# Performance work log

Measured on AMD Instinct MI355X. Metric: run time of the kernel, lower is better.

## Reference

```python
import jax, jax.numpy as jnp
import numpy as np
import math

B, N, D_MODEL, D_QK, D_V = 8, 2048, 512, 64, 64
NEG_INF = float('-inf')

def setup_inputs() -> dict:
    key = jax.random.key(0)
    k1, k2, k3, k4, k5 = jax.random.split(key, 5)
    mask = jax.random.randint(k1, (B, N, N), 0, 2).astype(bool)
    x_key_value = jax.random.normal(k2, (B, N, D_MODEL), dtype=jnp.float32)
    wk = jax.random.normal(k3, (D_MODEL, D_QK), dtype=jnp.float32) * 0.02
    wq = jax.random.normal(k4, (D_MODEL, D_QK), dtype=jnp.float32) * 0.02
    wv = jax.random.normal(k5, (D_MODEL, D_V), dtype=jnp.float32) * 0.02
    return {"mask": mask, "x_key_value": x_key_value, "wk": wk, "wq": wq, "wv": wv}

def reference(mask, x_key_value, wk, wq, wv):
    # self-attention: x_query defaults to x_key_value
    div = math.sqrt(wk.shape[1])
    k = x_key_value @ wk          # [n, j, d_qk]
    q = x_key_value @ wq          # [n, i, d_qk]
    v = x_key_value @ wv          # [n, j, d_v]
    mat = jnp.einsum('nik,njk->nij', q, k) / div
    mat = jnp.where(mask, mat, NEG_INF)
    portion = jax.nn.softmax(mat, axis=2)
    return jnp.einsum('nij,njk->nik', portion, v)
```

## Files before the change

### kernel.cpp

```cpp
#include <hip/hip_runtime.h>
#include <hip/hip_bf16.h>

typedef __attribute__((ext_vector_type(8))) short bf16x8;
typedef __attribute__((ext_vector_type(4))) float f32x4;
typedef __hip_bfloat16 bf16;

#define BATCH 8
#define SEQ   2048
#define DMODEL 512
#define DHEAD 64
#define ROWS (BATCH * SEQ)
#define SCALE_LOG2 0.1803368801f

static __device__ inline short f2bf(float f) {
    union { __hip_bfloat16 h; short s; } u;
    u.h = __float2bfloat16(f);
    return u.s;
}

__global__ __launch_bounds__(256) void transpose_w_kernel(
    const float* __restrict__ wq, const float* __restrict__ wk,
    const float* __restrict__ wv, bf16* __restrict__ wt)
{
    const int s  = blockIdx.x / 8;
    const int kt = blockIdx.x % 8;
    const float* w = (s == 0) ? wq : ((s == 1) ? wk : wv);

    __shared__ float Ts[64][68];

    const int tid = threadIdx.x;
    int nr = tid >> 4;
    int n4 = (tid & 15) * 4;
#pragma unroll
    for (int p = 0; p < 4; ++p) {
        int k = 16 * p + nr;
        float4 v = *(const float4*)(w + (size_t)(kt * 64 + k) * DHEAD + n4);
        Ts[k][n4] = v.x; Ts[k][n4 + 1] = v.y; Ts[k][n4 + 2] = v.z; Ts[k][n4 + 3] = v.w;
    }
    __syncthreads();
#pragma unroll
    for (int p = 0; p < 2; ++p) {
        int cc = tid + p * 256;
        int n = cc >> 3;
        int kk = (cc & 7) * 8;
        bf16x8 o;
#pragma unroll
        for (int e = 0; e < 8; ++e) o[e] = f2bf(Ts[kk + e][n]);
        *(bf16x8*)(wt + (size_t)(s * 64 + n) * DMODEL + kt * 64 + kk) = o;
    }
}

__global__ __launch_bounds__(512, 4) void proj_kernel(
    const float* __restrict__ x, const bf16* __restrict__ wt,
    bf16* __restrict__ Q, bf16* __restrict__ K, bf16* __restrict__ Vt)
{
    const int r0 = blockIdx.x * 32;
    const int tid = threadIdx.x;
    const int lane = tid & 63;
    const int wid = tid >> 6;
    const int strip = wid & 1;
    const int cq = wid >> 1;
    const int l15 = lane & 15;
    const int quad = lane >> 4;

    __shared__ __align__(8) bf16 Vs[64][36];

    f32x4 acc[3] = {};

    const float* xp = x + (size_t)(r0 + 16 * strip + l15) * DMODEL + quad * 8;

    float4 xa = *(const float4*)(xp);
    float4 xb = *(const float4*)(xp + 4);
    float4 xc = *(const float4*)(xp + 32);
    float4 xd = *(const float4*)(xp + 36);

    for (int k0 = 0; k0 < DMODEL; k0 += 64) {
        bf16x8 a0, a1;
        a0[0] = f2bf(xa.x); a0[1] = f2bf(xa.y); a0[2] = f2bf(xa.z); a0[3] = f2bf(xa.w);
        a0[4] = f2bf(xb.x); a0[5] = f2bf(xb.y); a0[6] = f2bf(xb.z); a0[7] = f2bf(xb.w);
        a1[0] = f2bf(xc.x); a1[1] = f2bf(xc.y); a1[2] = f2bf(xc.z); a1[3] = f2bf(xc.w);
        a1[4] = f2bf(xd.x); a1[5] = f2bf(xd.y); a1[6] = f2bf(xd.z); a1[7] = f2bf(xd.w);

        if (k0 + 64 < DMODEL) {
            xa = *(const float4*)(xp + k0 + 64);
            xb = *(const float4*)(xp + k0 + 68);
            xc = *(const float4*)(xp + k0 + 96);
            xd = *(const float4*)(xp + k0 + 100);
        }

#pragma unroll
        for (int g = 0; g < 3; ++g) {
            int n = 16 * (3 * cq + g) + l15;
            const bf16* wp = wt + (size_t)n * DMODEL + k0 + quad * 8;
            bf16x8 b0 = *(const bf16x8*)(wp);
            bf16x8 b1 = *(const bf16x8*)(wp + 32);
            acc[g] = __builtin_amdgcn_mfma_f32_16x16x32_bf16(a0, b0, acc[g], 0, 0, 0);
            acc[g] = __builtin_amdgcn_mfma_f32_16x16x32_bf16(a1, b1, acc[g], 0, 0, 0);
        }
    }

#pragma unroll
    for (int g = 0; g < 3; ++g) {
        int ng = 16 * (3 * cq + g) + l15;
        int sel = ng >> 6;
        int col = ng & 63;
#pragma unroll
        for (int r = 0; r < 4; ++r) {
            int rowl = 16 * strip + quad * 4 + r;
            int row = r0 + rowl;
            union { __hip_bfloat16 h; bf16 b; } u;
            u.h = __float2bfloat16(acc[g][r]);
            if (sel == 0)      Q[(size_t)row * DHEAD + col] = u.b;
            else if (sel == 1) K[(size_t)row * DHEAD + col] = u.b;
            else               Vs[col][rowl] = u.b;
        }
    }
    __syncthreads();

    {
        int d = tid >> 3;
        int j4 = (tid & 7) * 4;
        int bb = r0 >> 11;
        int j0 = r0 & (SEQ - 1);
        uint2 payload = *(const uint2*)(&Vs[d][j4]);
        *(uint2*)(Vt + ((size_t)(bb * DHEAD + d)) * SEQ + j0 + j4) = payload;
    }
}

__global__ __launch_bounds__(256, 4) void flash_kernel(
    const bf16* __restrict__ Q, const bf16* __restrict__ K,
    const bf16* __restrict__ Vt, const int* __restrict__ mask,
    float* __restrict__ out)
{
    const int b = blockIdx.x;
    const int q0 = blockIdx.y * 16;
    const int tid = threadIdx.x;
    const int lane = tid & 63;
    const int wid = tid >> 6;
    const int l15 = lane & 15;
    const int quad = lane >> 4;

    __shared__ __align__(16) bf16 Ps[4][16][72];
    __shared__ float Om[4][16][64];
    __shared__ float Lw[4][16];

    const bf16* qp = Q + ((size_t)(b * SEQ + q0 + l15)) * DHEAD + quad * 8;
    bf16x8 aQ0 = *(const bf16x8*)(qp);
    bf16x8 aQ1 = *(const bf16x8*)(qp + 32);

    f32x4 oacc[4] = {};
    float lsum[4] = {0.f, 0.f, 0.f, 0.f};

    const int* mp = mask + ((size_t)(b * SEQ + q0 + quad * 4)) * SEQ;
    const int jbase = wid * (SEQ / 4);

    int mpre[16];
#pragma unroll
    for (int c = 0; c < 4; ++c)
#pragma unroll
        for (int r = 0; r < 4; ++r)
            mpre[c * 4 + r] = mp[(size_t)r * SEQ + jbase + 16 * c + l15];

    for (int jt = 0; jt < 8; ++jt) {
        const int j0 = jbase + jt * 64;

        f32x4 sacc[4] = {};
#pragma unroll
        for (int c = 0; c < 4; ++c) {
            const bf16* kp = K + ((size_t)(b * SEQ + j0 + 16 * c + l15)) * DHEAD + quad * 8;
            bf16x8 b0 = *(const bf16x8*)(kp);
            bf16x8 b1 = *(const bf16x8*)(kp + 32);
            sacc[c] = __builtin_amdgcn_mfma_f32_16x16x32_bf16(aQ0, b0, sacc[c], 0, 0, 0);
            sacc[c] = __builtin_amdgcn_mfma_f32_16x16x32_bf16(aQ1, b1, sacc[c], 0, 0, 0);
        }

        float pv[4][4];
#pragma unroll
        for (int c = 0; c < 4; ++c)
#pragma unroll
            for (int r = 0; r < 4; ++r) {
                float e = exp2f(sacc[c][r] * SCALE_LOG2);
                float p = mpre[c * 4 + r] ? e : 0.0f;
                pv[c][r] = p;
                lsum[r] += p;
            }

        if (jt < 7) {
#pragma unroll
            for (int c = 0; c < 4; ++c)
#pragma unroll
                for (int r = 0; r < 4; ++r)
                    mpre[c * 4 + r] = mp[(size_t)r * SEQ + j0 + 64 + 16 * c + l15];
        }

#pragma unroll
        for (int c = 0; c < 4; ++c)
#pragma unroll
            for (int r = 0; r < 4; ++r) {
                union { __hip_bfloat16 h; bf16 b; } u;
                u.h = __float2bfloat16(pv[c][r]);
                Ps[wid][quad * 4 + r][16 * c + l15] = u.b;
            }

        bf16x8 aP0 = *(const bf16x8*)(&Ps[wid][l15][quad * 8]);
        bf16x8 aP1 = *(const bf16x8*)(&Ps[wid][l15][32 + quad * 8]);
#pragma unroll
        for (int c = 0; c < 4; ++c) {
            const bf16* vp = Vt + ((size_t)b * DHEAD + 16 * c + l15) * SEQ + j0 + quad * 8;
            bf16x8 v0 = *(const bf16x8*)(vp);
            bf16x8 v1 = *(const bf16x8*)(vp + 32);
            oacc[c] = __builtin_amdgcn_mfma_f32_16x16x32_bf16(aP0, v0, oacc[c], 0, 0, 0);
            oacc[c] = __builtin_amdgcn_mfma_f32_16x16x32_bf16(aP1, v1, oacc[c], 0, 0, 0);
        }
    }

#pragma unroll
    for (int r = 0; r < 4; ++r) {
        lsum[r] += __shfl_xor(lsum[r], 1);
        lsum[r] += __shfl_xor(lsum[r], 2);
        lsum[r] += __shfl_xor(lsum[r], 4);
        lsum[r] += __shfl_xor(lsum[r], 8);
    }

#pragma unroll
    for (int c = 0; c < 4; ++c)
#pragma unroll
        for (int r = 0; r < 4; ++r)
            Om[wid][quad * 4 + r][16 * c + l15] = oacc[c][r];
    if (l15 == 0) {
#pragma unroll
        for (int r = 0; r < 4; ++r) Lw[wid][quad * 4 + r] = lsum[r];
    }
    __syncthreads();

    {
        int row = tid >> 4;
        int c0 = (tid & 15) * 4;
        float L = Lw[0][row] + Lw[1][row] + Lw[2][row] + Lw[3][row];
        float invL = 1.0f / L;
        float4 o;
        float* op = (float*)&o;
#pragma unroll
        for (int e = 0; e < 4; ++e) {
            op[e] = (Om[0][row][c0 + e] + Om[1][row][c0 + e] +
                     Om[2][row][c0 + e] + Om[3][row][c0 + e]) * invL;
        }
        *(float4*)(out + ((size_t)(b * SEQ + q0 + row)) * DHEAD + c0) = o;
    }
}

extern "C" void kernel_launch(void* const* d_in, const int* in_sizes, int n_in,
                              void* d_out, int out_size, void* d_ws, size_t ws_size,
                              hipStream_t stream)
{
    const int*   mask = (const int*)d_in[0];
    const float* x    = (const float*)d_in[1];
    const float* wk   = (const float*)d_in[2];
    const float* wq   = (const float*)d_in[3];
    const float* wv   = (const float*)d_in[4];
    float* out = (float*)d_out;

    bf16* Qb = (bf16*)d_ws;
    bf16* Kb = Qb + (size_t)ROWS * DHEAD;
    bf16* Vt = Kb + (size_t)ROWS * DHEAD;
    bf16* Wt = Vt + (size_t)BATCH * DHEAD * SEQ;

    transpose_w_kernel<<<dim3(24), 256, 0, stream>>>(wq, wk, wv, Wt);
    proj_kernel<<<dim3(ROWS / 32), 512, 0, stream>>>(x, Wt, Qb, Kb, Vt);
    flash_kernel<<<dim3(BATCH, SEQ / 16), 256, 0, stream>>>(Qb, Kb, Vt, mask, out);
}
```

Baseline: 314.4 us.

## Pack int mask into bitmask in a prepass and read bits in flash kernel

Adds a pre-kernel that ballots the int32 mask into 64-bit words, so the flash kernel loads a few bitmask words per thread up front instead of streaming int mask values every tile. The goal is to make the flash kernel's mask traffic tiny and take the mask loads out of its inner loop. The full int mask still has to be read once by the pack kernel, which adds one launch and a workspace buffer. The projection kernel also interleaves its block order across batches and double-buffers its x prefetch two tiles ahead.

After: 322.5 us. 2.6% more time.

```diff
diff --git a/kernel.cpp b/kernel.cpp
--- a/kernel.cpp
+++ b/kernel.cpp
@@ -4,6 +4,7 @@
 typedef __attribute__((ext_vector_type(8))) short bf16x8;
 typedef __attribute__((ext_vector_type(4))) float f32x4;
 typedef __hip_bfloat16 bf16;
+typedef unsigned long long ull;
 
 #define BATCH 8
 #define SEQ   2048
@@ -18,6 +19,38 @@
     return u.s;
 }
 
+__global__ __launch_bounds__(256) void pack_mask_kernel(
+    const int* __restrict__ mask, ull* __restrict__ pm)
+{
+    const int wgl = (blockIdx.x * 256 + threadIdx.x) >> 6;
+    const int lane = threadIdx.x & 63;
+    const uint4* src = (const uint4*)mask;
+    const size_t cbase = (size_t)wgl * 32;
+
+    for (int it = 0; it < 8; ++it) {
+        size_t c0 = cbase + it * 4;
+        uint4 v0 = src[(c0 + 0) * 64 + lane];
+        uint4 v1 = src[(c0 + 1) * 64 + lane];
+        uint4 v2 = src[(c0 + 2) * 64 + lane];
+        uint4 v3 = src[(c0 + 3) * 64 + lane];
+        ull b00 = __ballot(v0.x != 0), b01 = __ballot(v0.y != 0);
+        ull b02 = __ballot(v0.z != 0), b03 = __ballot(v0.w != 0);
+        ull b10 = __ballot(v1.x != 0), b11 = __ballot(v1.y != 0);
+        ull b12 = __ballot(v1.z != 0), b13 = __ballot(v1.w != 0);
+        ull b20 = __ballot(v2.x != 0), b21 = __ballot(v2.y != 0);
+        ull b22 = __ballot(v2.z != 0), b23 = __ballot(v2.w != 0);
+        ull b30 = __ballot(v3.x != 0), b31 = __ballot(v3.y != 0);
+        ull b32 = __ballot(v3.z != 0), b33 = __ballot(v3.w != 0);
+        if (lane == 0) {
+            ull* d = pm + c0 * 4;
+            d[0] = b00; d[1] = b01; d[2]  = b02; d[3]  = b03;
+            d[4] = b10; d[5] = b11; d[6]  = b12; d[7]  = b13;
+            d[8] = b20; d[9] = b21; d[10] = b22; d[11] = b23;
+            d[12] = b30; d[13] = b31; d[14] = b32; d[15] = b33;
+        }
+    }
+}
+
 __global__ __launch_bounds__(256) void transpose_w_kernel(
     const float* __restrict__ wq, const float* __restrict__ wk,
     const float* __restrict__ wv, bf16* __restrict__ wt)
@@ -54,7 +87,9 @@
     const float* __restrict__ x, const bf16* __restrict__ wt,
     bf16* __restrict__ Q, bf16* __restrict__ K, bf16* __restrict__ Vt)
 {
-    const int r0 = blockIdx.x * 32;
+    const int bb = blockIdx.x & 7;
+    const int tt = blockIdx.x >> 3;
+    const int r0 = bb * SEQ + tt * 32;
     const int tid = threadIdx.x;
     const int lane = tid & 63;
     const int wid = tid >> 6;
@@ -69,23 +104,26 @@
 
     const float* xp = x + (size_t)(r0 + 16 * strip + l15) * DMODEL + quad * 8;
 
-    float4 xa = *(const float4*)(xp);
-    float4 xb = *(const float4*)(xp + 4);
-    float4 xc = *(const float4*)(xp + 32);
-    float4 xd = *(const float4*)(xp + 36);
-
+    float4 A0[4], A1[4];
+    A0[0] = *(const float4*)(xp + 0);  A0[1] = *(const float4*)(xp + 4);
+    A0[2] = *(const float4*)(xp + 32); A0[3] = *(const float4*)(xp + 36);
+    A1[0] = *(const float4*)(xp + 64); A1[1] = *(const float4*)(xp + 68);
+    A1[2] = *(const float4*)(xp + 96); A1[3] = *(const float4*)(xp + 100);
+
+#pragma unroll
     for (int k0 = 0; k0 < DMODEL; k0 += 64) {
+        float4* cur = ((k0 >> 6) & 1) ? A1 : A0;
         bf16x8 a0, a1;
-        a0[0] = f2bf(xa.x); a0[1] = f2bf(xa.y); a0[2] = f2bf(xa.z); a0[3] = f2bf(xa.w);
-        a0[4] = f2bf(xb.x); a0[5] = f2bf(xb.y); a0[6] = f2bf(xb.z); a0[7] = f2bf(xb.w);
-        a1[0] = f2bf(xc.x); a1[1] = f2bf(xc.y); a1[2] = f2bf(xc.z); a1[3] = f2bf(xc.w);
-        a1[4] = f2bf(xd.x); a1[5] = f2bf(xd.y); a1[6] = f2bf(xd.z); a1[7] = f2bf(xd.w);
-
-        if (k0 + 64 < DMODEL) {
-            xa = *(const float4*)(xp + k0 + 64);
-            xb = *(const float4*)(xp + k0 + 68);
-            xc = *(const float4*)(xp + k0 + 96);
-            xd = *(const float4*)(xp + k0 + 100);
+        a0[0] = f2bf(cur[0].x); a0[1] = f2bf(cur[0].y); a0[2] = f2bf(cur[0].z); a0[3] = f2bf(cur[0].w);
+        a0[4] = f2bf(cur[1].x); a0[5] = f2bf(cur[1].y); a0[6] = f2bf(cur[1].z); a0[7] = f2bf(cur[1].w);
+        a1[0] = f2bf(cur[2].x); a1[1] = f2bf(cur[2].y); a1[2] = f2bf(cur[2].z); a1[3] = f2bf(cur[2].w);
+        a1[4] = f2bf(cur[3].x); a1[5] = f2bf(cur[3].y); a1[6] = f2bf(cur[3].z); a1[7] = f2bf(cur[3].w);
+
+        if (k0 + 128 < DMODEL) {
+            cur[0] = *(const float4*)(xp + k0 + 128);
+            cur[1] = *(const float4*)(xp + k0 + 132);
+            cur[2] = *(const float4*)(xp + k0 + 160);
+            cur[3] = *(const float4*)(xp + k0 + 164);
         }
 
 #pragma unroll
@@ -120,8 +158,7 @@
     {
         int d = tid >> 3;
         int j4 = (tid & 7) * 4;
-        int bb = r0 >> 11;
-        int j0 = r0 & (SEQ - 1);
+        int j0 = tt * 32;
         uint2 payload = *(const uint2*)(&Vs[d][j4]);
         *(uint2*)(Vt + ((size_t)(bb * DHEAD + d)) * SEQ + j0 + j4) = payload;
     }
@@ -129,7 +166,7 @@
 
 __global__ __launch_bounds__(256, 4) void flash_kernel(
     const bf16* __restrict__ Q, const bf16* __restrict__ K,
-    const bf16* __restrict__ Vt, const int* __restrict__ mask,
+    const bf16* __restrict__ Vt, const ull* __restrict__ pm,
     float* __restrict__ out)
 {
     const int b = blockIdx.x;
@@ -144,6 +181,18 @@
     __shared__ float Om[4][16][64];
     __shared__ float Lw[4][16];
 
+    ull mw[2][4];
+    {
+        const int sh = l15 >> 2;
+#pragma unroll
+        for (int ch = 0; ch < 2; ++ch)
+#pragma unroll
+            for (int r = 0; r < 4; ++r) {
+                size_t row = (size_t)(b * SEQ + q0 + quad * 4 + r);
+                mw[ch][r] = pm[(row * 8 + wid * 2 + ch) * 4 + (l15 & 3)] >> sh;
+            }
+    }
+
     const bf16* qp = Q + ((size_t)(b * SEQ + q0 + l15)) * DHEAD + quad * 8;
     bf16x8 aQ0 = *(const bf16x8*)(qp);
     bf16x8 aQ1 = *(const bf16x8*)(qp + 32);
@@ -151,17 +200,12 @@
     f32x4 oacc[4] = {};
     float lsum[4] = {0.f, 0.f, 0.f, 0.f};
 
-    const int* mp = mask + ((size_t)(b * SEQ + q0 + quad * 4)) * SEQ;
     const int jbase = wid * (SEQ / 4);
 
-    int mpre[16];
-#pragma unroll
-    for (int c = 0; c < 4; ++c)
-#pragma unroll
-        for (int r = 0; r < 4; ++r)
-            mpre[c * 4 + r] = mp[(size_t)r * SEQ + jbase + 16 * c + l15];
-
+#pragma unroll
     for (int jt = 0; jt < 8; ++jt) {
+        const int ch = jt >> 2;
+        const int s = jt & 3;
         const int j0 = jbase + jt * 64;
 
         f32x4 sacc[4] = {};
@@ -180,18 +224,11 @@
 #pragma unroll
             for (int r = 0; r < 4; ++r) {
                 float e = exp2f(sacc[c][r] * SCALE_LOG2);
-                float p = mpre[c * 4 + r] ? e : 0.0f;
+                unsigned bit = (unsigned)(mw[ch][r] >> (16 * s + 4 * c)) & 1u;
+                float p = bit ? e : 0.0f;
                 pv[c][r] = p;
                 lsum[r] += p;
             }
-
-        if (jt < 7) {
-#pragma unroll
-            for (int c = 0; c < 4; ++c)
-#pragma unroll
-                for (int r = 0; r < 4; ++r)
-                    mpre[c * 4 + r] = mp[(size_t)r * SEQ + j0 + 64 + 16 * c + l15];
-        }
 
 #pragma unroll
         for (int c = 0; c < 4; ++c)
@@ -264,8 +301,10 @@
     bf16* Kb = Qb + (size_t)ROWS * DHEAD;
     bf16* Vt = Kb + (size_t)ROWS * DHEAD;
     bf16* Wt = Vt + (size_t)BATCH * DHEAD * SEQ;
-
+    ull*  pm = (ull*)(Wt + 3 * 64 * DMODEL);
+
+    pack_mask_kernel<<<dim3(1024), 256, 0, stream>>>(mask, pm);
     transpose_w_kernel<<<dim3(24), 256, 0, stream>>>(wq, wk, wv, Wt);
     proj_kernel<<<dim3(ROWS / 32), 512, 0, stream>>>(x, Wt, Qb, Kb, Vt);
-    flash_kernel<<<dim3(BATCH, SEQ / 16), 256, 0, stream>>>(Qb, Kb, Vt, mask, out);
-}
+    flash_kernel<<<dim3(BATCH, SEQ / 16), 256, 0, stream>>>(Qb, Kb, Vt, pm, out);
+}
```
